# Performance work log

Hardware: AMD Instinct MI355X
Metric: run time of the kernel (lower is better)

Reference implementation:

```python
import jax, jax.numpy as jnp
import numpy as np
from jax import lax

K_NN = 16      # neighbors used by compute_knn_distance
ANCHOR_K = 64  # config['anchor_k']


def _knn_dist_vec(pts):
    """compute_knn_distance for one object: mean offset vector to K_NN nearest neighbors.
    pts: (N, 3) -> (N, 3)"""
    sq = jnp.sum(pts * pts, axis=-1)                      # (N,)
    d2 = sq[:, None] + sq[None, :] - 2.0 * (pts @ pts.T)  # (N, N) squared dists
    n = pts.shape[0]
    d2 = d2 + jnp.eye(n, dtype=pts.dtype) * 1e10          # exclude self
    _, idx = lax.top_k(-d2, K_NN)                          # (N, K_NN) nearest indices
    neigh = pts[idx]                                       # (N, K_NN, 3)
    return jnp.mean(neigh - pts[:, None, :], axis=1)       # (N, 3)


def _fps(pts, k):
    """Farthest point sampling for one object. pts: (N, 3) -> (k,) int32 indices."""
    d0 = jnp.sum((pts - pts[0]) ** 2, axis=-1)             # dist to seed point 0

    def step(min_d, _):
        idx = jnp.argmax(min_d)
        d = jnp.sum((pts - pts[idx]) ** 2, axis=-1)
        return jnp.minimum(min_d, d), idx

    _, idxs = lax.scan(step, d0, None, length=k - 1)
    return jnp.concatenate([jnp.zeros((1,), dtype=idxs.dtype), idxs])


def setup_inputs() -> dict:
    key = jax.random.key(0)
    k1, k2, k3, k4 = jax.random.split(key, 4)
    B, N_obj, N_v = 4, 8, 2048
    positions = jax.random.normal(k1, (B, N_obj, N_v, 3), dtype=jnp.float32)
    velocities = jax.random.normal(k2, (B, N_obj, N_v, 3), dtype=jnp.float32)
    physics_params = jax.random.uniform(k3, (B, N_obj, 3), dtype=jnp.float32)
    # reference pose at t=0: nearby but distinct so rel_pos is nontrivial
    ref_positions = positions + 0.05 * jax.random.normal(k4, (B, N_obj, N_v, 3), dtype=jnp.float32)
    return {"positions": positions, "velocities": velocities,
            "physics_params": physics_params, "ref_positions": ref_positions}


def reference(positions, velocities, physics_params, ref_positions):
    B, N_obj, N_v, _ = positions.shape
    flat = positions.reshape(B * N_obj, N_v, 3)

    # pairwise KNN distance feature per point
    dist_vec = jax.vmap(_knn_dist_vec)(flat).reshape(B, N_obj, N_v, 3)

    # iterative FPS anchor sampling (vectorized over all B*N_obj objects)
    anchors = jax.vmap(lambda p: _fps(p, ANCHOR_K))(flat).reshape(B, N_obj, ANCHOR_K)

    rel_pos = positions - ref_positions

    # multi-field gather at anchor indices (torch.gather on dim=2)
    gather = lambda f: jnp.take_along_axis(f, anchors[..., None], axis=2)
    anchor_dist = gather(dist_vec)       # (B, N_obj, K, 3)
    anchor_vel = gather(velocities)      # (B, N_obj, K, 3)
    anchor_rel = gather(rel_pos)         # (B, N_obj, K, 3)

    phys = jnp.broadcast_to(physics_params[:, :, None, :], (B, N_obj, ANCHOR_K, 3))
    query = jnp.concatenate([anchor_dist, anchor_vel, anchor_rel, phys], axis=-1)  # (B, N_obj, K, 12)
    return query
```

## Files before the change

### kernel.cpp

```cpp
#include <hip/hip_runtime.h>
#include <stdint.h>

#define NPTS 2048
#define KNN  16
#define AK   64
#define TPB  256
#define FPT  (NPTS / TPB)
#define KPL  (NPTS / 64)

typedef unsigned long long u64;
typedef unsigned int u32;
#define UMAX 0xFFFFFFFFFFFFFFFFull

__device__ __forceinline__ float sq3(float x, float y, float z) {
    return __fadd_rn(__fadd_rn(__fmul_rn(x, x), __fmul_rn(y, y)), __fmul_rn(z, z));
}

template <int CTRL>
__device__ __forceinline__ u64 dpp64(u64 k) {
    const int lo = __builtin_amdgcn_update_dpp((int)(u32)k, (int)(u32)k,
                                               CTRL, 0xF, 0xF, false);
    const int hi = __builtin_amdgcn_update_dpp((int)(u32)(k >> 32),
                                               (int)(u32)(k >> 32),
                                               CTRL, 0xF, 0xF, false);
    return ((u64)(u32)hi << 32) | (u32)lo;
}

__device__ __forceinline__ void swap16_pair(u64 k, u64& a, u64& b) {
#if __has_builtin(__builtin_amdgcn_permlane16_swap)
    const u32 lo = (u32)k, hi = (u32)(k >> 32);
    const auto rl = __builtin_amdgcn_permlane16_swap(lo, lo, false, false);
    const auto rh = __builtin_amdgcn_permlane16_swap(hi, hi, false, false);
    a = ((u64)(u32)rh[0] << 32) | (u32)rl[0];
    b = ((u64)(u32)rh[1] << 32) | (u32)rl[1];
#else
    a = (u64)__shfl_xor((long long)k, 16, 64);
    b = a;
#endif
}

__device__ __forceinline__ void swap32_pair(u64 k, u64& a, u64& b) {
#if __has_builtin(__builtin_amdgcn_permlane32_swap)
    const u32 lo = (u32)k, hi = (u32)(k >> 32);
    const auto rl = __builtin_amdgcn_permlane32_swap(lo, lo, false, false);
    const auto rh = __builtin_amdgcn_permlane32_swap(hi, hi, false, false);
    a = ((u64)(u32)rh[0] << 32) | (u32)rl[0];
    b = ((u64)(u32)rh[1] << 32) | (u32)rl[1];
#else
    a = (u64)__shfl_xor((long long)k, 32, 64);
    b = a;
#endif
}

__device__ __forceinline__ u64 wave_max64(u64 k) {
    u64 o, a, b;
    o = dpp64<0xB1>(k);  if (o > k) k = o;
    o = dpp64<0x4E>(k);  if (o > k) k = o;
    o = dpp64<0x141>(k); if (o > k) k = o;
    o = dpp64<0x140>(k); if (o > k) k = o;
    swap16_pair(k, a, b); if (a > k) k = a; if (b > k) k = b;
    swap32_pair(k, a, b); if (a > k) k = a; if (b > k) k = b;
    return k;
}

__device__ __forceinline__ u64 wave_min64(u64 k) {
    u64 o, a, b;
    o = dpp64<0xB1>(k);  if (o < k) k = o;
    o = dpp64<0x4E>(k);  if (o < k) k = o;
    o = dpp64<0x141>(k); if (o < k) k = o;
    o = dpp64<0x140>(k); if (o < k) k = o;
    swap16_pair(k, a, b); if (a < k) k = a; if (b < k) k = b;
    swap32_pair(k, a, b); if (a < k) k = a; if (b < k) k = b;
    return k;
}

__global__ __launch_bounds__(TPB) void fps_kernel(const float* __restrict__ pos,
                                                  int* __restrict__ anchors) {
    const int obj = blockIdx.x;
    const int t = threadIdx.x;
    const int wid = t >> 6, lane = t & 63;

    __shared__ float4 sP[NPTS];
    __shared__ u64 skey[8];
    __shared__ float4 scrd[8];
    __shared__ int sAnc[AK];

    const float* pts = pos + (size_t)obj * NPTS * 3;
    float px[FPT], py[FPT], pz[FPT], mind[FPT];
    #pragma unroll
    for (int i = 0; i < FPT; i++) {
        const int j = t + i * TPB;
        const float x = pts[j * 3 + 0];
        const float y = pts[j * 3 + 1];
        const float z = pts[j * 3 + 2];
        px[i] = x; py[i] = y; pz[i] = z;
        sP[j] = make_float4(x, y, z, 0.f);
    }
    if (t == 0) sAnc[0] = 0;
    __syncthreads();

    u64 key;
    {
        const float4 c0 = sP[0];
        float bv = -1.0f; u32 bj = 0;
        #pragma unroll
        for (int i = 0; i < FPT; i++) {
            const float d2 = sq3(__fsub_rn(px[i], c0.x), __fsub_rn(py[i], c0.y),
                                 __fsub_rn(pz[i], c0.z));
            mind[i] = d2;
            if (d2 > bv) { bv = d2; bj = (u32)(t + i * TPB); }
        }
        key = ((u64)__float_as_uint(bv) << 32) | (u32)(~bj);
    }

    #pragma unroll 1
    for (int s = 1; s < AK; s++) {
        const u64 wk = wave_max64(key);
        const int side = (s & 1) * 4;
        if (lane == 0) {
            const int widx = (int)(~(u32)wk);
            skey[side + wid] = wk;
            scrd[side + wid] = sP[widx];
        }
        __syncthreads();
        u64 ka = skey[side + 0];
        float4 ca = scrd[side + 0];
        { const u64 k1 = skey[side + 1]; const float4 q = scrd[side + 1];
          if (k1 > ka) { ka = k1; ca = q; } }
        { const u64 k2 = skey[side + 2]; const float4 q = scrd[side + 2];
          if (k2 > ka) { ka = k2; ca = q; } }
        { const u64 k3 = skey[side + 3]; const float4 q = scrd[side + 3];
          if (k3 > ka) { ka = k3; ca = q; } }
        if (t == 0) sAnc[s] = (int)(~(u32)ka);
        if (s == AK - 1) break;

        float bv = -1.0f; u32 bj = 0;
        #pragma unroll
        for (int i = 0; i < FPT; i++) {
            const float d2 = sq3(__fsub_rn(px[i], ca.x), __fsub_rn(py[i], ca.y),
                                 __fsub_rn(pz[i], ca.z));
            const float nm = fminf(mind[i], d2);
            mind[i] = nm;
            if (nm > bv) { bv = nm; bj = (u32)(t + i * TPB); }
        }
        key = ((u64)__float_as_uint(bv) << 32) | (u32)(~bj);
    }

    __syncthreads();
    if (t < AK) anchors[obj * AK + t] = sAnc[t];
}

__global__ __launch_bounds__(TPB) void knn_gather_kernel(
    const float* __restrict__ pos, const float* __restrict__ vel,
    const float* __restrict__ phys, const float* __restrict__ refp,
    const int* __restrict__ anchors, float* __restrict__ out) {
    const int t = threadIdx.x;
    const int wid = t >> 6, lane = t & 63;
    const int g = blockIdx.x * 4 + wid;
    const int obj = g >> 6;

    __shared__ float4 sP[NPTS];
    const float* pts = pos + (size_t)obj * NPTS * 3;
    #pragma unroll
    for (int i = 0; i < FPT; i++) {
        const int j = t + i * TPB;
        const float x = pts[j * 3 + 0];
        const float y = pts[j * 3 + 1];
        const float z = pts[j * 3 + 2];
        sP[j] = make_float4(x, y, z, sq3(x, y, z));
    }
    const int a = anchors[g];
    __syncthreads();

    const float4 ca = sP[a];
    const float ax = ca.x, ay = ca.y, az = ca.z;
    const float sqa = ca.w;

    u64 k[KPL];
    #pragma unroll
    for (int i = 0; i < KPL; i++) {
        const int j = lane + i * 64;
        const float4 p = sP[j];
        const float dot = __fadd_rn(
            __fadd_rn(__fmul_rn(ax, p.x), __fmul_rn(ay, p.y)), __fmul_rn(az, p.z));
        const float d2 = __fsub_rn(__fadd_rn(sqa, p.w), __fmul_rn(2.0f, dot));
        u32 bb = __float_as_uint(d2);
        bb ^= (bb & 0x80000000u) ? 0xFFFFFFFFu : 0x80000000u;
        k[i] = (j == a) ? UMAX : (((u64)bb << 32) | (u32)j);
    }

    u64 c0 = UMAX, c1 = UMAX, c2 = UMAX, c3 = UMAX;
    #pragma unroll
    for (int i = 0; i < KPL; i++) c0 = (k[i] < c0) ? k[i] : c0;
    #pragma unroll
    for (int i = 0; i < KPL; i++) {
        const u64 v = (k[i] > c0) ? k[i] : UMAX; c1 = (v < c1) ? v : c1;
    }
    #pragma unroll
    for (int i = 0; i < KPL; i++) {
        const u64 v = (k[i] > c1) ? k[i] : UMAX; c2 = (v < c2) ? v : c2;
    }
    #pragma unroll
    for (int i = 0; i < KPL; i++) {
        const u64 v = (k[i] > c2) ? k[i] : UMAX; c3 = (v < c3) ? v : c3;
    }

    float accx = 0.f, accy = 0.f, accz = 0.f;
    u64 thr = 0;
    float4 cw;
    {
        const u64 w = wave_min64(c0);
        cw = sP[(int)(u32)w];
        if (c0 == w) { thr = c0; c0 = c1; c1 = c2; c2 = c3; c3 = UMAX; }
    }
    #pragma unroll 1
    for (int r = 1; r < KNN; r++) {
        if (c0 == UMAX) {
            #pragma unroll
            for (int i = 0; i < KPL; i++) {
                const u64 v = (k[i] > thr) ? k[i] : UMAX; c0 = (v < c0) ? v : c0;
            }
            #pragma unroll
            for (int i = 0; i < KPL; i++) {
                const u64 v = (k[i] > c0) ? k[i] : UMAX; c1 = (v < c1) ? v : c1;
            }
            #pragma unroll
            for (int i = 0; i < KPL; i++) {
                const u64 v = (k[i] > c1) ? k[i] : UMAX; c2 = (v < c2) ? v : c2;
            }
            #pragma unroll
            for (int i = 0; i < KPL; i++) {
                const u64 v = (k[i] > c2) ? k[i] : UMAX; c3 = (v < c3) ? v : c3;
            }
        }
        const u64 w = wave_min64(c0);
        const float4 cn = sP[(int)(u32)w];
        accx = __fadd_rn(accx, __fsub_rn(cw.x, ax));
        accy = __fadd_rn(accy, __fsub_rn(cw.y, ay));
        accz = __fadd_rn(accz, __fsub_rn(cw.z, az));
        cw = cn;
        if (c0 == w) {
            thr = c0; c0 = c1; c1 = c2; c2 = c3; c3 = UMAX;
        }
    }
    accx = __fadd_rn(accx, __fsub_rn(cw.x, ax));
    accy = __fadd_rn(accy, __fsub_rn(cw.y, ay));
    accz = __fadd_rn(accz, __fsub_rn(cw.z, az));

    if (lane == 0) {
        float* o = out + (size_t)g * 12;
        o[0] = __fmul_rn(accx, 0.0625f);
        o[1] = __fmul_rn(accy, 0.0625f);
        o[2] = __fmul_rn(accz, 0.0625f);
        const size_t base = (size_t)obj * NPTS * 3 + (size_t)a * 3;
        o[3] = vel[base + 0];
        o[4] = vel[base + 1];
        o[5] = vel[base + 2];
        o[6] = __fsub_rn(pos[base + 0], refp[base + 0]);
        o[7] = __fsub_rn(pos[base + 1], refp[base + 1]);
        o[8] = __fsub_rn(pos[base + 2], refp[base + 2]);
        const float* ph = phys + (size_t)obj * 3;
        o[9]  = ph[0];
        o[10] = ph[1];
        o[11] = ph[2];
    }
}

extern "C" void kernel_launch(void* const* d_in, const int* in_sizes, int n_in,
                              void* d_out, int out_size, void* d_ws, size_t ws_size,
                              hipStream_t stream) {
    const float* pos  = (const float*)d_in[0];
    const float* vel  = (const float*)d_in[1];
    const float* phys = (const float*)d_in[2];
    const float* refp = (const float*)d_in[3];
    float* out = (float*)d_out;

    const int n_obj = in_sizes[2] / 3;
    int* anchors = (int*)d_ws;

    fps_kernel<<<n_obj, TPB, 0, stream>>>(pos, anchors);
    knn_gather_kernel<<<n_obj * AK / 4, TPB, 0, stream>>>(pos, vel, phys, refp,
                                                          anchors, out);
}
```

Before: 110.9 us.

## Fuse FPS and KNN-gather into one kernel with progress-flag streaming

Merges the FPS and KNN/gather kernels into one launch. The first n_obj blocks run FPS and publish anchor indices in chunks of 8 (as u16) with a release-store progress counter. The remaining blocks each handle 4 anchors, spin-waiting on that counter before starting their KNN work, so KNN overlaps with the still-running FPS. This removes the kernel boundary serialisation but adds a memset launch and relies on the FPS blocks being scheduled, with a risk of deadlock if consumer blocks occupy all CUs first.

```diff
diff --git a/kernel.cpp b/kernel.cpp
--- a/kernel.cpp
+++ b/kernel.cpp
@@ -10,6 +10,7 @@
 
 typedef unsigned long long u64;
 typedef unsigned int u32;
+typedef unsigned short u16;
 #define UMAX 0xFFFFFFFFFFFFFFFFull
 
 __device__ __forceinline__ float sq3(float x, float y, float z) {
@@ -74,92 +75,104 @@
     return k;
 }
 
-__global__ __launch_bounds__(TPB) void fps_kernel(const float* __restrict__ pos,
-                                                  int* __restrict__ anchors) {
-    const int obj = blockIdx.x;
+__global__ __launch_bounds__(TPB) void fused_kernel(
+    const float* __restrict__ pos, const float* __restrict__ vel,
+    const float* __restrict__ phys, const float* __restrict__ refp,
+    u16* __restrict__ anc16, int* __restrict__ prog,
+    float* __restrict__ out, int n_obj) {
+    const int b = blockIdx.x;
     const int t = threadIdx.x;
     const int wid = t >> 6, lane = t & 63;
 
     __shared__ float4 sP[NPTS];
     __shared__ u64 skey[8];
     __shared__ float4 scrd[8];
-    __shared__ int sAnc[AK];
-
-    const float* pts = pos + (size_t)obj * NPTS * 3;
-    float px[FPT], py[FPT], pz[FPT], mind[FPT];
-    #pragma unroll
-    for (int i = 0; i < FPT; i++) {
-        const int j = t + i * TPB;
-        const float x = pts[j * 3 + 0];
-        const float y = pts[j * 3 + 1];
-        const float z = pts[j * 3 + 2];
-        px[i] = x; py[i] = y; pz[i] = z;
-        sP[j] = make_float4(x, y, z, 0.f);
-    }
-    if (t == 0) sAnc[0] = 0;
-    __syncthreads();
-
-    u64 key;
-    {
-        const float4 c0 = sP[0];
-        float bv = -1.0f; u32 bj = 0;
+    __shared__ int sAq[4];
+
+    if (b < n_obj) {
+        const int obj = b;
+        const float* pts = pos + (size_t)obj * NPTS * 3;
+        float px[FPT], py[FPT], pz[FPT], mind[FPT];
         #pragma unroll
         for (int i = 0; i < FPT; i++) {
-            const float d2 = sq3(__fsub_rn(px[i], c0.x), __fsub_rn(py[i], c0.y),
-                                 __fsub_rn(pz[i], c0.z));
-            mind[i] = d2;
-            if (d2 > bv) { bv = d2; bj = (u32)(t + i * TPB); }
-        }
-        key = ((u64)__float_as_uint(bv) << 32) | (u32)(~bj);
-    }
-
-    #pragma unroll 1
-    for (int s = 1; s < AK; s++) {
-        const u64 wk = wave_max64(key);
-        const int side = (s & 1) * 4;
-        if (lane == 0) {
-            const int widx = (int)(~(u32)wk);
-            skey[side + wid] = wk;
-            scrd[side + wid] = sP[widx];
+            const int j = t + i * TPB;
+            const float x = pts[j * 3 + 0];
+            const float y = pts[j * 3 + 1];
+            const float z = pts[j * 3 + 2];
+            px[i] = x; py[i] = y; pz[i] = z;
+            sP[j] = make_float4(x, y, z, 0.f);
         }
         __syncthreads();
-        u64 ka = skey[side + 0];
-        float4 ca = scrd[side + 0];
-        { const u64 k1 = skey[side + 1]; const float4 q = scrd[side + 1];
-          if (k1 > ka) { ka = k1; ca = q; } }
-        { const u64 k2 = skey[side + 2]; const float4 q = scrd[side + 2];
-          if (k2 > ka) { ka = k2; ca = q; } }
-        { const u64 k3 = skey[side + 3]; const float4 q = scrd[side + 3];
-          if (k3 > ka) { ka = k3; ca = q; } }
-        if (t == 0) sAnc[s] = (int)(~(u32)ka);
-        if (s == AK - 1) break;
-
-        float bv = -1.0f; u32 bj = 0;
-        #pragma unroll
-        for (int i = 0; i < FPT; i++) {
-            const float d2 = sq3(__fsub_rn(px[i], ca.x), __fsub_rn(py[i], ca.y),
-                                 __fsub_rn(pz[i], ca.z));
-            const float nm = fminf(mind[i], d2);
-            mind[i] = nm;
-            if (nm > bv) { bv = nm; bj = (u32)(t + i * TPB); }
-        }
-        key = ((u64)__float_as_uint(bv) << 32) | (u32)(~bj);
-    }
-
-    __syncthreads();
-    if (t < AK) anchors[obj * AK + t] = sAnc[t];
-}
-
-__global__ __launch_bounds__(TPB) void knn_gather_kernel(
-    const float* __restrict__ pos, const float* __restrict__ vel,
-    const float* __restrict__ phys, const float* __restrict__ refp,
-    const int* __restrict__ anchors, float* __restrict__ out) {
-    const int t = threadIdx.x;
-    const int wid = t >> 6, lane = t & 63;
-    const int g = blockIdx.x * 4 + wid;
-    const int obj = g >> 6;
-
-    __shared__ float4 sP[NPTS];
+
+        u64 ap0 = 0, ap1 = 0;
+        #define PUSH_AID(v) { ap0 = (ap0 >> 16) | (ap1 << 48); \
+                              ap1 = (ap1 >> 16) | ((u64)(u16)(v) << 48); }
+        PUSH_AID(0);
+
+        u64 key;
+        {
+            const float4 c0 = sP[0];
+            float bv = -1.0f; u32 bj = 0;
+            #pragma unroll
+            for (int i = 0; i < FPT; i++) {
+                const float d2 = sq3(__fsub_rn(px[i], c0.x), __fsub_rn(py[i], c0.y),
+                                     __fsub_rn(pz[i], c0.z));
+                mind[i] = d2;
+                if (d2 > bv) { bv = d2; bj = (u32)(t + i * TPB); }
+            }
+            key = ((u64)__float_as_uint(bv) << 32) | (u32)(~bj);
+        }
+
+        #pragma unroll 1
+        for (int s = 1; s < AK; s++) {
+            const u64 wk = wave_max64(key);
+            const int side = (s & 1) * 4;
+            if (lane == 0) {
+                const int widx = (int)(~(u32)wk);
+                skey[side + wid] = wk;
+                scrd[side + wid] = sP[widx];
+            }
+            __syncthreads();
+            u64 ka = skey[side + 0];
+            float4 ca = scrd[side + 0];
+            { const u64 k1 = skey[side + 1]; const float4 q = scrd[side + 1];
+              if (k1 > ka) { ka = k1; ca = q; } }
+            { const u64 k2 = skey[side + 2]; const float4 q = scrd[side + 2];
+              if (k2 > ka) { ka = k2; ca = q; } }
+            { const u64 k3 = skey[side + 3]; const float4 q = scrd[side + 3];
+              if (k3 > ka) { ka = k3; ca = q; } }
+
+            const int aid = (int)(~(u32)ka);
+            PUSH_AID(aid);
+            if ((s & 7) == 7 && t == 0) {
+                const int4 v = make_int4((int)(u32)ap0, (int)(u32)(ap0 >> 32),
+                                         (int)(u32)ap1, (int)(u32)(ap1 >> 32));
+                *(int4*)(anc16 + obj * AK + (s - 7)) = v;
+                __threadfence();
+                __hip_atomic_store(&prog[obj], s + 1, __ATOMIC_RELEASE,
+                                   __HIP_MEMORY_SCOPE_AGENT);
+            }
+            if (s == AK - 1) break;
+
+            float bv = -1.0f; u32 bj = 0;
+            #pragma unroll
+            for (int i = 0; i < FPT; i++) {
+                const float d2 = sq3(__fsub_rn(px[i], ca.x), __fsub_rn(py[i], ca.y),
+                                     __fsub_rn(pz[i], ca.z));
+                const float nm = fminf(mind[i], d2);
+                mind[i] = nm;
+                if (nm > bv) { bv = nm; bj = (u32)(t + i * TPB); }
+            }
+            key = ((u64)__float_as_uint(bv) << 32) | (u32)(~bj);
+        }
+        return;
+    }
+
+    const int g4 = b - n_obj;
+    const int obj = g4 >> 4;
+    const int q = g4 & 15;
+    const int g = obj * AK + q * 4 + wid;
+
     const float* pts = pos + (size_t)obj * NPTS * 3;
     #pragma unroll
     for (int i = 0; i < FPT; i++) {
@@ -169,8 +182,16 @@
         const float z = pts[j * 3 + 2];
         sP[j] = make_float4(x, y, z, sq3(x, y, z));
     }
-    const int a = anchors[g];
+    if (t == 0) {
+        const int need = q * 4 + 4;
+        while (__hip_atomic_load(&prog[obj], __ATOMIC_ACQUIRE,
+                                 __HIP_MEMORY_SCOPE_AGENT) < need)
+            __builtin_amdgcn_s_sleep(4);
+        const u16* ap = anc16 + obj * AK + q * 4;
+        sAq[0] = ap[0]; sAq[1] = ap[1]; sAq[2] = ap[2]; sAq[3] = ap[3];
+    }
     __syncthreads();
+    const int a = sAq[wid];
 
     const float4 ca = sP[a];
     const float ax = ca.x, ay = ca.y, az = ca.z;
@@ -276,9 +297,11 @@
     float* out = (float*)d_out;
 
     const int n_obj = in_sizes[2] / 3;
-    int* anchors = (int*)d_ws;
-
-    fps_kernel<<<n_obj, TPB, 0, stream>>>(pos, anchors);
-    knn_gather_kernel<<<n_obj * AK / 4, TPB, 0, stream>>>(pos, vel, phys, refp,
-                                                          anchors, out);
-}
+    u16* anc16 = (u16*)d_ws;
+    int* prog = (int*)((char*)d_ws + n_obj * AK * sizeof(u16));
+
+    hipMemsetAsync(prog, 0, n_obj * sizeof(int), stream);
+
+    fused_kernel<<<n_obj * 17, TPB, 0, stream>>>(pos, vel, phys, refp,
+                                                 anc16, prog, out, n_obj);
+}
```

After: 150.8 us. +36.0%, slower.

## Fuse FPS into KNN-gather blocks by recomputing FPS prefix per block

Applied to the files above, without the earlier changes.

Merges the two kernels into one. Each of the 16 blocks per object redundantly runs farthest point sampling only as far as the 4 anchors it needs, then does the KNN and gather work for those anchors. This removes the second launch, the global anchor round trip and the serial FPS phase running on only 32 blocks. In exchange it repeats FPS work: late blocks run up to 63 steps, so total FPS compute grows about eightfold and block durations become uneven.

```diff
diff --git a/kernel.cpp b/kernel.cpp
--- a/kernel.cpp
+++ b/kernel.cpp
@@ -10,6 +10,7 @@
 
 typedef unsigned long long u64;
 typedef unsigned int u32;
+typedef unsigned short u16;
 #define UMAX 0xFFFFFFFFFFFFFFFFull
 
 __device__ __forceinline__ float sq3(float x, float y, float z) {
@@ -74,16 +75,19 @@
     return k;
 }
 
-__global__ __launch_bounds__(TPB) void fps_kernel(const float* __restrict__ pos,
-                                                  int* __restrict__ anchors) {
-    const int obj = blockIdx.x;
+__global__ __launch_bounds__(TPB) void fused_kernel(
+    const float* __restrict__ pos, const float* __restrict__ vel,
+    const float* __restrict__ phys, const float* __restrict__ refp,
+    float* __restrict__ out, int n_obj) {
+    const int b = blockIdx.x;
+    const int obj = b >> 4;
+    const int q = b & 15;
     const int t = threadIdx.x;
     const int wid = t >> 6, lane = t & 63;
 
     __shared__ float4 sP[NPTS];
     __shared__ u64 skey[8];
     __shared__ float4 scrd[8];
-    __shared__ int sAnc[AK];
 
     const float* pts = pos + (size_t)obj * NPTS * 3;
     float px[FPT], py[FPT], pz[FPT], mind[FPT];
@@ -94,10 +98,11 @@
         const float y = pts[j * 3 + 1];
         const float z = pts[j * 3 + 2];
         px[i] = x; py[i] = y; pz[i] = z;
-        sP[j] = make_float4(x, y, z, 0.f);
-    }
-    if (t == 0) sAnc[0] = 0;
+        sP[j] = make_float4(x, y, z, sq3(x, y, z));
+    }
     __syncthreads();
+
+    u32 a0 = 0, a1 = 0, a2 = 0, a3 = 0;
 
     u64 key;
     {
@@ -113,8 +118,9 @@
         key = ((u64)__float_as_uint(bv) << 32) | (u32)(~bj);
     }
 
+    const int smax = q * 4 + 3;
     #pragma unroll 1
-    for (int s = 1; s < AK; s++) {
+    for (int s = 1; s <= smax; s++) {
         const u64 wk = wave_max64(key);
         const int side = (s & 1) * 4;
         if (lane == 0) {
@@ -125,14 +131,20 @@
         __syncthreads();
         u64 ka = skey[side + 0];
         float4 ca = scrd[side + 0];
-        { const u64 k1 = skey[side + 1]; const float4 q = scrd[side + 1];
-          if (k1 > ka) { ka = k1; ca = q; } }
-        { const u64 k2 = skey[side + 2]; const float4 q = scrd[side + 2];
-          if (k2 > ka) { ka = k2; ca = q; } }
-        { const u64 k3 = skey[side + 3]; const float4 q = scrd[side + 3];
-          if (k3 > ka) { ka = k3; ca = q; } }
-        if (t == 0) sAnc[s] = (int)(~(u32)ka);
-        if (s == AK - 1) break;
+        { const u64 k1 = skey[side + 1]; const float4 qq = scrd[side + 1];
+          if (k1 > ka) { ka = k1; ca = qq; } }
+        { const u64 k2 = skey[side + 2]; const float4 qq = scrd[side + 2];
+          if (k2 > ka) { ka = k2; ca = qq; } }
+        { const u64 k3 = skey[side + 3]; const float4 qq = scrd[side + 3];
+          if (k3 > ka) { ka = k3; ca = qq; } }
+
+        const u32 aid = ~(u32)ka;
+        const int r = s - q * 4;
+        if (r == 0) a0 = aid;
+        else if (r == 1) a1 = aid;
+        else if (r == 2) a2 = aid;
+        else if (r == 3) a3 = aid;
+        if (s == smax) break;
 
         float bv = -1.0f; u32 bj = 0;
         #pragma unroll
@@ -146,31 +158,12 @@
         key = ((u64)__float_as_uint(bv) << 32) | (u32)(~bj);
     }
 
-    __syncthreads();
-    if (t < AK) anchors[obj * AK + t] = sAnc[t];
-}
-
-__global__ __launch_bounds__(TPB) void knn_gather_kernel(
-    const float* __restrict__ pos, const float* __restrict__ vel,
-    const float* __restrict__ phys, const float* __restrict__ refp,
-    const int* __restrict__ anchors, float* __restrict__ out) {
-    const int t = threadIdx.x;
-    const int wid = t >> 6, lane = t & 63;
-    const int g = blockIdx.x * 4 + wid;
-    const int obj = g >> 6;
-
-    __shared__ float4 sP[NPTS];
-    const float* pts = pos + (size_t)obj * NPTS * 3;
-    #pragma unroll
-    for (int i = 0; i < FPT; i++) {
-        const int j = t + i * TPB;
-        const float x = pts[j * 3 + 0];
-        const float y = pts[j * 3 + 1];
-        const float z = pts[j * 3 + 2];
-        sP[j] = make_float4(x, y, z, sq3(x, y, z));
-    }
-    const int a = anchors[g];
-    __syncthreads();
+    u32 av = a0;
+    if (wid == 1) av = a1;
+    else if (wid == 2) av = a2;
+    else if (wid == 3) av = a3;
+    const int a = (int)av;
+    const int g = obj * AK + q * 4 + wid;
 
     const float4 ca = sP[a];
     const float ax = ca.x, ay = ca.y, az = ca.z;
@@ -276,9 +269,7 @@
     float* out = (float*)d_out;
 
     const int n_obj = in_sizes[2] / 3;
-    int* anchors = (int*)d_ws;
-
-    fps_kernel<<<n_obj, TPB, 0, stream>>>(pos, anchors);
-    knn_gather_kernel<<<n_obj * AK / 4, TPB, 0, stream>>>(pos, vel, phys, refp,
-                                                          anchors, out);
-}
+
+    fused_kernel<<<n_obj * 16, TPB, 0, stream>>>(pos, vel, phys, refp,
+                                                 out, n_obj);
+}
```

Measured after the change: 117.0 us. +5.5%, slower.
